# Performance work log

Hardware: AMD Instinct MI355X
Metric: run time of the kernel (lower is better)

## Reference

```python
import jax, jax.numpy as jnp
import numpy as np

DX, DY, MR, MBAR, NT, B, GOUT = 16, 8, 64, 256, 9, 4, 64
HX, EX, HRNN, HB = 1024, 512, 512, 2048
BB_IN = 1 + EX + HRNN


def setup_inputs() -> dict:
    key = jax.random.key(0)
    ks = jax.random.split(key, 12)
    total = (NT - 1) * MBAR + 1  # 2049 hidden-process time points
    X = jax.random.randint(ks[0], (B, total, DX), 0, 50).astype(jnp.float32)  # molecule counts
    Y = jax.random.normal(ks[1], (B, NT, DY), dtype=jnp.float32)
    # R: cumulative integrated reaction rates (non-decreasing in time)
    R = jnp.cumsum(jax.random.uniform(ks[2], (B, total, MR), dtype=jnp.float32) * 0.01, axis=1)
    stoich = (jax.random.randint(ks[3], (DX, MR), 0, 3) - 1).astype(jnp.float32)  # entries in {-1,0,1}
    times_t = jnp.linspace(0.0, 8.0, NT).astype(jnp.float32)
    times_tau = jnp.linspace(0.0, 1.0, MBAR).astype(jnp.float32)
    sc = lambda k, sh: jax.random.normal(k, sh, dtype=jnp.float32) * np.float32(1.0 / np.sqrt(sh[0]))
    Wx1, bx1 = sc(ks[4], (DX, HX)), jnp.zeros(HX, jnp.float32)
    Wx2, bx2 = sc(ks[5], (HX, EX)), jnp.zeros(EX, jnp.float32)
    Wih = sc(ks[6], (DY, HRNN))
    Whh = sc(ks[7], (HRNN, HRNN))
    bh = jnp.zeros(HRNN, jnp.float32)
    Wb1, bb1 = sc(ks[8], (BB_IN, HB)), jnp.zeros(HB, jnp.float32)
    Wb2, bb2 = sc(ks[9], (HB, GOUT)), jnp.zeros(GOUT, jnp.float32)
    return dict(X=X, Y=Y, R=R, stoich=stoich, times_t=times_t, times_tau=times_tau,
                Wx1=Wx1, bx1=bx1, Wx2=Wx2, bx2=bx2, Wih=Wih, Whh=Whh, bh=bh,
                Wb1=Wb1, bb1=bb1, Wb2=Wb2, bb2=bb2, k=1, k_prime=1, q=0, q_prime=1)


def reference(X, Y, R, stoich, times_t, times_tau,
              Wx1, bx1, Wx2, bx2, Wih, Whh, bh, Wb1, bb1, Wb2, bb2,
              k, k_prime, q, q_prime):
    """stochastic_integral_vectorized: gather displaced states, run the
    martingale network forward on base and displaced states, masked
    accumulation weighted by rate increments. Returns [GOUT]."""
    m_bar = times_tau.shape[0]
    base = k_prime * m_bar

    # --- Y encoder (Elman RNN over the observation slice, final hidden state) ---
    Yslice = Y[q, k + 1:, :]                       # [T_rem, DY]
    def rnn_step(h, y):
        return jnp.tanh(y @ Wih + h @ Whh + bh), None
    eY, _ = jax.lax.scan(rnn_step, jnp.zeros(Whh.shape[0], X.dtype), Yslice)  # [HRNN]

    # --- batched martingale forward: t [N], Xb [N, DX] -> [N, GOUT] ---
    def batched_forward(t, Xb):
        eX = jnp.tanh(Xb @ Wx1 + bx1) @ Wx2 + bx2          # [N, EX]
        eYb = jnp.broadcast_to(eY, (Xb.shape[0], eY.shape[0]))
        inp = jnp.concatenate([t[:, None], eX, eYb], axis=1)  # [N, 1+EX+HRNN]
        return jnp.tanh(inp @ Wb1 + bb1) @ Wb2 + bb2       # [N, GOUT]

    Xbase = X[q_prime, base:base + m_bar, :]               # [M_bar, DX]
    t = times_t[k] + times_tau                              # [M_bar]
    nn = batched_forward(t, Xbase)                          # [M_bar, GOUT]

    mr = stoich.shape[1]
    X_disp = Xbase[None, :, :] + stoich.T[:, None, :]       # [MR, M_bar, DX]
    valid = jnp.all(X_disp >= 0, axis=-1)                   # [MR, M_bar]
    nn_disp = batched_forward(jnp.tile(t, mr),
                              X_disp.reshape(mr * m_bar, -1)).reshape(mr, m_bar, -1)

    R_delta = R[q_prime, base + 1:base + m_bar + 1, :] - R[q_prime, base:base + m_bar, :]  # [M_bar, MR]
    si = jnp.einsum('jmg,mj,jm->g', nn_disp - nn[None], R_delta, valid.astype(nn.dtype))
    return si
```

## Files before the change

kernel.cpp:

```cpp
#include <hip/hip_runtime.h>
#include <math.h>

#define DXc   16
#define MRc   64
#define MBARc 256
#define NTc   9
#define DYc   8
#define HXc   1024
#define EXc   512
#define HRc   512
#define HBc   2048
#define GOUTc 64
#define TOTc  2049

using bf16x8 = __attribute__((ext_vector_type(8))) short;
using f32x4  = __attribute__((ext_vector_type(4))) float;

typedef unsigned int u32;
typedef u32 __attribute__((address_space(1))) gbl_u32;
typedef u32 __attribute__((address_space(3))) lds_u32;

__device__ __forceinline__ float fast_tanh(float x){
    float e = __expf(2.0f * x);
    return 1.0f - 2.0f / (e + 1.0f);
}

__device__ __forceinline__ short f2bf(float f){
    unsigned u = __builtin_bit_cast(unsigned, f);
    u = (u + 0x7FFFu + ((u >> 16) & 1u)) >> 16;
    return (short)u;
}

__device__ __forceinline__ void gld_lds16(const short* g, short* l){
    __builtin_amdgcn_global_load_lds((const gbl_u32*)g, (lds_u32*)l, 16, 0, 0);
}

__global__ void prep_kernel(const float* __restrict__ stoich, const float* __restrict__ Wx1,
                            const float* __restrict__ Wx2, const float* __restrict__ Wb1,
                            const float* __restrict__ X, const float* __restrict__ R,
                            const float* __restrict__ bx1, const float* __restrict__ bx2,
                            const int* kpptr, const int* qpptr,
                            float* __restrict__ SW, short* __restrict__ Wx2a,
                            short* __restrict__ Wb1p, float* __restrict__ XW,
                            float* __restrict__ T1, float* __restrict__ wrow,
                            float* __restrict__ hb0, float* __restrict__ dacc,
                            float* __restrict__ outz, float* __restrict__ eXb,
                            float* __restrict__ Z2Bacc, int* __restrict__ cnt){
    int b = blockIdx.x, tid = threadIdx.x;
    if (b < 256){
        int idx = b * 256 + tid;
        int j = idx >> 10, c = idx & 1023;
        float acc = 0.f;
        #pragma unroll
        for (int d = 0; d < DXc; ++d) acc += stoich[d * MRc + j] * Wx1[d * HXc + c];
        SW[idx] = acc;
    } else if (b < 512){
        size_t grp = (size_t)(b - 256) * 256 + tid;
        int lane = grp & 63;
        size_t t2 = grp >> 6;
        int kt = t2 & 15, mt = t2 >> 4;
        int c  = mt * 16 + (lane & 15);
        int e0 = kt * 32 + ((lane >> 4) << 3);
        short o8[8];
        #pragma unroll
        for (int jj = 0; jj < 8; ++jj) o8[jj] = f2bf(Wx2[(size_t)c * EXc + e0 + jj]);
        *(bf16x8*)(Wx2a + grp * 8) = *(bf16x8*)o8;
    } else if (b < 1024){
        size_t grp = (size_t)(b - 512) * 256 + tid;
        int lane = grp & 63;
        size_t t2 = grp >> 6;
        int kt = t2 & 15, nt = t2 >> 4;
        int n  = nt * 16 + (lane & 15);
        int k0 = kt * 32 + ((lane >> 4) << 3);
        short o8[8];
        #pragma unroll
        for (int jj = 0; jj < 8; ++jj) o8[jj] = f2bf(Wb1[(size_t)(1 + k0 + jj) * HBc + n]);
        *(bf16x8*)(Wb1p + grp * 8) = *(bf16x8*)o8;
    } else if (b < 2048){
        int idx = (b - 1024) * 256 + tid;
        int m = idx >> 10, c = idx & 1023;
        int base = kpptr[0] * MBARc;
        const float* xr = X + ((size_t)qpptr[0] * TOTc + base + m) * DXc;
        float acc = bx1[c];
        #pragma unroll
        for (int d = 0; d < DXc; ++d) acc += xr[d] * Wx1[d * HXc + c];
        XW[idx] = acc;
        T1[idx] = fast_tanh(acc);
    } else if (b < 2112){
        int j = b - 2048, m = tid;
        int base = kpptr[0] * MBARc;
        int qp = qpptr[0];
        const float* xr = X + ((size_t)qp * TOTc + base + m) * DXc;
        bool valid = true;
        #pragma unroll
        for (int d = 0; d < DXc; ++d) valid = valid && (xr[d] + stoich[d * MRc + j] >= 0.f);
        size_t rb = (size_t)qp * TOTc * MRc;
        float rd = R[rb + (size_t)(base + 1 + m) * MRc + j] - R[rb + (size_t)(base + m) * MRc + j];
        wrow[j * MBARc + m] = valid ? rd : 0.f;
    } else if (b == 2112){
        hb0[tid] = 0.f; hb0[tid + 256] = 0.f;
        #pragma unroll
        for (int l = 0; l < 8; ++l) dacc[tid + l * 256] = 0.f;
        if (tid < GOUTc) outz[tid] = 0.f;
        if (tid == 0) cnt[0] = 0;
    } else if (b < 2625){
        int idx = (b - 2113) * 256 + tid;
        eXb[idx] = bx2[idx & 511];
    } else {
        Z2Bacc[(size_t)(b - 2625) * 256 + tid] = 0.f;
    }
}

#define MMGRID(aa, bb) {                                                       \
    _Pragma("unroll") for (int i_ = 0; i_ < 4; ++i_)                           \
        _Pragma("unroll") for (int j_ = 0; j_ < 4; ++j_)                       \
            acc[i_][j_] = __builtin_amdgcn_mfma_f32_16x16x32_bf16(aa[i_], bb[j_], acc[i_][j_], 0, 0, 0); }

__device__ __forceinline__ void stage32(const short* __restrict__ Ap, const short* __restrict__ Bp,
                                        short* As, short* Bs,
                                        int at0, int bt0, int s, int KTOT, int wave, int lane){
    #pragma unroll
    for (int c = 0; c < 4; ++c){
        int ci = wave * 4 + c;
        int half = ci >> 3;
        int t    = ci & 7;
        const short* src = half ? (Bp + ((size_t)(bt0 + t) * KTOT + s) * 512 + lane * 8)
                                : (Ap + ((size_t)(at0 + t) * KTOT + s) * 512 + lane * 8);
        short* dst = (half ? Bs : As) + t * 512;
        gld_lds16(src, dst);
    }
}

#define STAGE_COMPUTE(As, Bs) {                                                       \
    bf16x8 af[4], bfr[4];                                                             \
    _Pragma("unroll") for (int i_ = 0; i_ < 4; ++i_)                                  \
        af[i_] = *(const bf16x8*)((As) + ((wm * 4 + i_) * 512) + lane * 8);           \
    _Pragma("unroll") for (int j_ = 0; j_ < 4; ++j_)                                  \
        bfr[j_] = *(const bf16x8*)((Bs) + ((wn * 4 + j_) * 512) + lane * 8);          \
    MMGRID(af, bfr); }

__global__ __launch_bounds__(256) void w12_act_ex_kernel(
    const short* __restrict__ Wx2a, const short* __restrict__ Wb1p,
    short* __restrict__ W12p,
    const float* __restrict__ XW, const float* __restrict__ T1,
    const float* __restrict__ SW, short* __restrict__ A1p,
    const float* __restrict__ Wx2, float* __restrict__ eXb){
    __shared__ __align__(16) short Asb[2][4096];
    __shared__ __align__(16) short Bsb[2][4096];
    int b = blockIdx.x, tid = threadIdx.x;
    if (b < 128){
        const int KTOT = 16, S = 16;
        int wave = tid >> 6, lane = tid & 63;
        int wm = wave >> 1, wn = wave & 1;
        int bx = b & 15, by = b >> 4;
        int quad = lane >> 4, llo = lane & 15;
        f32x4 acc[4][4];
        #pragma unroll
        for (int i = 0; i < 4; ++i)
            #pragma unroll
            for (int j = 0; j < 4; ++j) acc[i][j] = (f32x4){0.f, 0.f, 0.f, 0.f};
        stage32(Wx2a, Wb1p, Asb[0], Bsb[0], by * 8, bx * 8, 0, KTOT, wave, lane);
        for (int s = 0; s < S; ++s){
            int buf = s & 1;
            __syncthreads();
            if (s + 1 < S)
                stage32(Wx2a, Wb1p, Asb[buf ^ 1], Bsb[buf ^ 1], by * 8, bx * 8, s + 1, KTOT, wave, lane);
            STAGE_COMPUTE(Asb[buf], Bsb[buf]);
        }
        #pragma unroll
        for (int j = 0; j < 4; ++j){
            int h = bx * 128 + wn * 64 + j * 16 + llo;
            #pragma unroll
            for (int i = 0; i < 4; ++i){
                #pragma unroll
                for (int r = 0; r < 4; ++r){
                    int c = by * 128 + wm * 64 + i * 16 + quad * 4 + r;
                    W12p[(((size_t)(h >> 4) * 32 + (c >> 5)) * 64 + ((c & 31) >> 3) * 16 + llo) * 8 + (c & 7)] =
                        f2bf(acc[i][j][r]);
                }
            }
        }
    } else if (b < 8320){
        size_t grp = (size_t)(b - 128) * 256 + tid;
        int lane = grp & 63;
        size_t t2 = grp >> 6;
        int kt = t2 & 31;
        int mt = (int)(t2 >> 5);
        int m  = mt * 16 + (lane & 15);
        int c0 = kt * 32 + ((lane >> 4) << 3);
        int j    = m >> 8;
        int mloc = m & 255;
        const float* xwr = XW + (size_t)mloc * HXc + c0;
        const float* t1r = T1 + (size_t)mloc * HXc + c0;
        const float* swr = SW + (size_t)j * HXc + c0;
        short o8[8];
        #pragma unroll
        for (int i = 0; i < 8; ++i)
            o8[i] = f2bf(fast_tanh(xwr[i] + swr[i]) - t1r[i]);
        *(bf16x8*)(A1p + grp * 8) = *(bf16x8*)o8;
    } else {
        __shared__ float t1s[8 * 128];
        int bb = b - 8320;
        int mg = bb & 31, eh = (bb >> 5) & 1, kq = bb >> 6;
        int m0 = mg * 8, e = eh * 256 + tid, k0 = kq * 128;
        #pragma unroll
        for (int l = 0; l < 4; ++l){
            int idx = tid + l * 256;
            t1s[idx] = T1[(size_t)(m0 + (idx >> 7)) * HXc + k0 + (idx & 127)];
        }
        __syncthreads();
        float acc[8] = {};
        #pragma unroll 4
        for (int kk = 0; kk < 128; ++kk){
            float wv = Wx2[(size_t)(k0 + kk) * EXc + e];
            #pragma unroll
            for (int mm = 0; mm < 8; ++mm) acc[mm] += t1s[mm * 128 + kk] * wv;
        }
        #pragma unroll
        for (int mm = 0; mm < 8; ++mm)
            atomicAdd(&eXb[(size_t)(m0 + mm) * EXc + e], acc[mm]);
    }
}

__global__ __launch_bounds__(512) void rnn_cy_kernel(
    const float* __restrict__ Y, const float* __restrict__ Wih,
    const float* __restrict__ Whh, const float* __restrict__ bh,
    const float* __restrict__ Wb1, const float* __restrict__ bb1,
    const int* kptr, const int* qptr,
    float* __restrict__ hb0, float* __restrict__ hb1,
    int* __restrict__ cnt, float* __restrict__ cY){
    __shared__ float hs[HRc];
    __shared__ float psum[8][64];
    __shared__ float ps2[2][256];
    int tid = threadIdx.x;
    int o = tid & 63, seg = tid >> 6;
    int b = blockIdx.x;
    int out = b * 64 + o;
    int k = kptr[0], q = qptr[0];
    hs[tid] = 0.f;
    __syncthreads();
    for (int s = 0; s < 8; ++s){
        float* dst = (s & 1) ? hb0 : hb1;
        if (s > 0){
            const float* src = (s & 1) ? hb1 : hb0;
            if (tid == 0){
                int guard = 0;
                while (__hip_atomic_load(cnt, __ATOMIC_ACQUIRE, __HIP_MEMORY_SCOPE_AGENT) < 8 * s
                       && ++guard < (1 << 26)) {}
            }
            __syncthreads();
            hs[tid] = __hip_atomic_load(src + tid, __ATOMIC_RELAXED, __HIP_MEMORY_SCOPE_AGENT);
            __syncthreads();
        }
        int t = k + 1 + s;
        if (t < NTc){
            int k0 = seg * 64;
            float a0 = 0.f, a1 = 0.f, a2 = 0.f, a3 = 0.f;
            #pragma unroll 4
            for (int kk = 0; kk < 64; kk += 4){
                a0 += hs[k0 + kk + 0] * Whh[(size_t)(k0 + kk + 0) * HRc + out];
                a1 += hs[k0 + kk + 1] * Whh[(size_t)(k0 + kk + 1) * HRc + out];
                a2 += hs[k0 + kk + 2] * Whh[(size_t)(k0 + kk + 2) * HRc + out];
                a3 += hs[k0 + kk + 3] * Whh[(size_t)(k0 + kk + 3) * HRc + out];
            }
            psum[seg][o] = (a0 + a1) + (a2 + a3);
            __syncthreads();
            if (seg == 0){
                float a = 0.f;
                #pragma unroll
                for (int r = 0; r < 8; ++r) a += psum[r][o];
                const float* y = Y + (q * NTc + t) * DYc;
                float z = bh[out];
                #pragma unroll
                for (int d = 0; d < DYc; ++d) z += y[d] * Wih[d * HRc + out];
                __hip_atomic_store(dst + out, fast_tanh(z + a), __ATOMIC_RELEASE, __HIP_MEMORY_SCOPE_AGENT);
            }
            __syncthreads();
        } else {
            if (seg == 0)
                __hip_atomic_store(dst + out, hs[out], __ATOMIC_RELEASE, __HIP_MEMORY_SCOPE_AGENT);
            __syncthreads();
        }
        if (tid == 0)
            __hip_atomic_fetch_add(cnt, 1, __ATOMIC_RELEASE, __HIP_MEMORY_SCOPE_AGENT);
    }
    if (tid == 0){
        int guard = 0;
        while (__hip_atomic_load(cnt, __ATOMIC_ACQUIRE, __HIP_MEMORY_SCOPE_AGENT) < 64
               && ++guard < (1 << 26)) {}
    }
    __syncthreads();
    hs[tid] = __hip_atomic_load(hb0 + tid, __ATOMIC_RELAXED, __HIP_MEMORY_SCOPE_AGENT);
    __syncthreads();
    int o2 = tid & 255, sg = tid >> 8;
    int h = b * 256 + o2;
    float acc = 0.f;
    int e0 = sg * 256;
    #pragma unroll 4
    for (int e = 0; e < 256; ++e)
        acc += hs[e0 + e] * Wb1[(size_t)(1 + EXc + e0 + e) * HBc + h];
    ps2[sg][o2] = acc;
    __syncthreads();
    if (sg == 0)
        cY[h] = bb1[h] + ps2[0][o2] + ps2[1][o2];
}

__global__ __launch_bounds__(256) void z2acc_kernel(const float* __restrict__ eXb,
                                                    const float* __restrict__ Wb1,
                                                    float* __restrict__ Z2Bacc){
    __shared__ float exs[8 * 256];
    int b = blockIdx.x, tid = threadIdx.x;
    int mg = b & 31, hh = (b >> 5) & 7, kq = b >> 8;
    int m0 = mg * 8, h = hh * 256 + tid, k0 = kq * 256;
    #pragma unroll
    for (int l = 0; l < 8; ++l){
        int idx = tid + l * 256;
        exs[idx] = eXb[(size_t)(m0 + (idx >> 8)) * EXc + k0 + (idx & 255)];
    }
    __syncthreads();
    float acc[8] = {};
    #pragma unroll 4
    for (int kk = 0; kk < 256; ++kk){
        float wv = Wb1[(size_t)(1 + k0 + kk) * HBc + h];
        #pragma unroll
        for (int mm = 0; mm < 8; ++mm) acc[mm] += exs[mm * 256 + kk] * wv;
    }
    #pragma unroll
    for (int mm = 0; mm < 8; ++mm)
        atomicAdd(&Z2Bacc[(size_t)(m0 + mm) * HBc + h], acc[mm]);
}

__global__ void tb_kernel(const float* __restrict__ Z2Bacc, const float* __restrict__ Wb1,
                          const float* __restrict__ cY, const float* __restrict__ times_t,
                          const float* __restrict__ times_tau, const int* kptr,
                          float* __restrict__ TB){
    int b = blockIdx.x, tid = threadIdx.x;
    int m = b >> 3, h = (b & 7) * 256 + tid;
    float tk = times_t[kptr[0]];
    size_t idx = (size_t)m * HBc + h;
    float z = Z2Bacc[idx] + (tk + times_tau[m]) * Wb1[h] + cY[h];
    TB[idx] = fast_tanh(z);
}

__device__ __forceinline__ void stage24(const short* __restrict__ Ap, const short* __restrict__ Bp,
                                        short* As, short* Bs,
                                        int at0, int bt0, int s, int wave, int lane){
    #pragma unroll
    for (int c = 0; c < 6; ++c){
        int ci = wave * 6 + c;
        const short* src;
        short* dst;
        if (ci < 8){
            src = Ap + ((size_t)(at0 + ci) * 32 + s) * 512 + lane * 8;
            dst = As + ci * 512;
        } else {
            int t = ci - 8;
            src = Bp + ((size_t)(bt0 + t) * 32 + s) * 512 + lane * 8;
            dst = Bs + t * 512;
        }
        gld_lds16(src, dst);
    }
}

__global__ __launch_bounds__(256, 2) void gemm_big(
    const short* __restrict__ Ap, const short* __restrict__ Bp,
    const float* __restrict__ TB, const float* __restrict__ wrow,
    float* __restrict__ dacc){
    const int S = 32;
    __shared__ __align__(16) short Asb[2][4096];
    __shared__ __align__(16) short Bsb[2][8192];
    int tid = threadIdx.x;
    int wave = tid >> 6, lane = tid & 63;
    int wm = wave >> 1, wn = wave & 1;
    int bm = blockIdx.x, bn = blockIdx.y;
    int quad = lane >> 4, llo = lane & 15;
    f32x4 acc[4][8];
    #pragma unroll
    for (int i = 0; i < 4; ++i)
        #pragma unroll
        for (int j = 0; j < 8; ++j) acc[i][j] = (f32x4){0.f, 0.f, 0.f, 0.f};
    stage24(Ap, Bp, Asb[0], Bsb[0], bm * 8, bn * 16, 0, wave, lane);
    for (int s = 0; s < S; ++s){
        int buf = s & 1;
        __syncthreads();
        if (s + 1 < S)
            stage24(Ap, Bp, Asb[buf ^ 1], Bsb[buf ^ 1], bm * 8, bn * 16, s + 1, wave, lane);
        {
            bf16x8 af[4], bfr[8];
            #pragma unroll
            for (int i = 0; i < 4; ++i)
                af[i] = *(const bf16x8*)(Asb[buf] + ((wm * 4 + i) * 512) + lane * 8);
            #pragma unroll
            for (int j = 0; j < 8; ++j)
                bfr[j] = *(const bf16x8*)(Bsb[buf] + ((wn * 8 + j) * 512) + lane * 8);
            #pragma unroll
            for (int i = 0; i < 4; ++i)
                #pragma unroll
                for (int j = 0; j < 8; ++j)
                    acc[i][j] = __builtin_amdgcn_mfma_f32_16x16x32_bf16(af[i], bfr[j], acc[i][j], 0, 0, 0);
        }
    }
    int nj[8];
    #pragma unroll
    for (int j = 0; j < 8; ++j) nj[j] = bn * 256 + wn * 128 + j * 16 + llo;
    float part[8] = {};
    #pragma unroll
    for (int i = 0; i < 4; ++i){
        #pragma unroll
        for (int r = 0; r < 4; ++r){
            int m = bm * 128 + wm * 64 + i * 16 + quad * 4 + r;
            float wr = wrow[m];
            const float* trow = TB + (size_t)(m & 255) * HBc;
            #pragma unroll
            for (int j = 0; j < 8; ++j){
                float tb  = trow[nj[j]];
                float tdz = fast_tanh(acc[i][j][r]);
                float num = tdz * (1.0f - tb * tb);
                float den = 1.0f + tb * tdz;
                part[j] += wr * num * __builtin_amdgcn_rcpf(den);
            }
        }
    }
    #pragma unroll
    for (int j = 0; j < 8; ++j){
        part[j] += __shfl_xor(part[j], 16);
        part[j] += __shfl_xor(part[j], 32);
    }
    __shared__ float redn[256];
    redn[tid] = 0.f;
    __syncthreads();
    if (lane < 16){
        #pragma unroll
        for (int j = 0; j < 8; ++j)
            atomicAdd(&redn[wn * 128 + j * 16 + llo], part[j]);
    }
    __syncthreads();
    atomicAdd(&dacc[bn * 256 + tid], redn[tid]);
}

__global__ void out_kernel(const float* __restrict__ dacc, const float* __restrict__ Wb2,
                           float* __restrict__ out){
    __shared__ float red[4][64];
    int tid = threadIdx.x;
    int g = tid & 63, seg = tid >> 6;
    int h0 = blockIdx.x * 256 + seg * 64;
    float s = 0.f;
    #pragma unroll 8
    for (int hh = 0; hh < 64; ++hh)
        s += dacc[h0 + hh] * Wb2[(size_t)(h0 + hh) * GOUTc + g];
    red[seg][g] = s;
    __syncthreads();
    if (tid < 64)
        atomicAdd(&out[tid], red[0][tid] + red[1][tid] + red[2][tid] + red[3][tid]);
}

extern "C" void kernel_launch(void* const* d_in, const int* in_sizes, int n_in,
                              void* d_out, int out_size, void* d_ws, size_t ws_size,
                              hipStream_t stream){
    const float* X         = (const float*)d_in[0];
    const float* Y         = (const float*)d_in[1];
    const float* R         = (const float*)d_in[2];
    const float* stoich    = (const float*)d_in[3];
    const float* times_t   = (const float*)d_in[4];
    const float* times_tau = (const float*)d_in[5];
    const float* Wx1 = (const float*)d_in[6];
    const float* bx1 = (const float*)d_in[7];
    const float* Wx2 = (const float*)d_in[8];
    const float* bx2 = (const float*)d_in[9];
    const float* Wih = (const float*)d_in[10];
    const float* Whh = (const float*)d_in[11];
    const float* bh  = (const float*)d_in[12];
    const float* Wb1 = (const float*)d_in[13];
    const float* bb1 = (const float*)d_in[14];
    const float* Wb2 = (const float*)d_in[15];
    const int* kp  = (const int*)d_in[17];
    const int* kpp = (const int*)d_in[18];
    const int* qp  = (const int*)d_in[19];
    const int* qpp = (const int*)d_in[20];
    float* out = (float*)d_out;

    float* ws     = (float*)d_ws;
    float* hb0    = ws;
    float* hb1    = ws + 512;
    float* cY     = ws + 1024;
    float* dacc   = ws + 3072;
    float* wrow   = ws + 5120;
    float* SW     = ws + 21504;
    float* XW     = ws + 87040;
    float* T1     = ws + 349184;
    float* eXb    = ws + 611328;
    float* TB     = ws + 742400;
    float* Z2Bacc = ws + 1266688;
    short* A1p    = (short*)(ws + 1790976);
    short* Wx2a   = (short*)(ws + 10179584);
    short* Wb1p   = (short*)(ws + 10441728);
    short* W12p   = (short*)(ws + 10966016);
    int*   cnt    = (int*)(ws + 12014592);

    prep_kernel      <<<4673, 256, 0, stream>>>(stoich, Wx1, Wx2, Wb1, X, R, bx1, bx2, kpp, qpp,
                                                SW, Wx2a, Wb1p, XW, T1, wrow, hb0, dacc, out,
                                                eXb, Z2Bacc, cnt);
    w12_act_ex_kernel<<<8832, 256, 0, stream>>>(Wx2a, Wb1p, W12p, XW, T1, SW, A1p, Wx2, eXb);
    rnn_cy_kernel    <<<8,    512, 0, stream>>>(Y, Wih, Whh, bh, Wb1, bb1, kp, qp, hb0, hb1, cnt, cY);
    z2acc_kernel     <<<512,  256, 0, stream>>>(eXb, Wb1, Z2Bacc);
    tb_kernel        <<<2048, 256, 0, stream>>>(Z2Bacc, Wb1, cY, times_t, times_tau, kp, TB);
    gemm_big         <<<dim3(128, 8), 256, 0, stream>>>(A1p, W12p, TB, wrow, dacc);
    out_kernel       <<<8,    256, 0, stream>>>(dacc, Wb2, out);
}
```

Baseline: 293.5 us.

## Merge RNN/cY kernel into W12 and activation kernel, memset Z2Bacc, raise gemm occupancy

The serial RNN recurrence and cY projection now run as the first 8 blocks of a combined kernel that also does the W12 GEMM, the eX partial product and the A1 activation packing, so the latency-bound recurrence overlaps with that bulk work instead of running as its own launch. The eX block range moves ahead of A1 packing, Z2Bacc zeroing moves from prep_kernel blocks to hipMemsetAsync, and gemm_big's launch bounds ask for 3 blocks per CU. The RNN blocks spin on a global counter, so they depend on all 8 being resident together; putting them first in the grid makes that likely but not certain. The higher occupancy target may force register spills in gemm_big.

```diff
diff --git a/kernel.cpp b/kernel.cpp
--- a/kernel.cpp
+++ b/kernel.cpp
@@ -45,7 +45,7 @@
                             float* __restrict__ T1, float* __restrict__ wrow,
                             float* __restrict__ hb0, float* __restrict__ dacc,
                             float* __restrict__ outz, float* __restrict__ eXb,
-                            float* __restrict__ Z2Bacc, int* __restrict__ cnt){
+                            int* __restrict__ cnt){
     int b = blockIdx.x, tid = threadIdx.x;
     if (b < 256){
         int idx = b * 256 + tid;
@@ -103,11 +103,9 @@
         for (int l = 0; l < 8; ++l) dacc[tid + l * 256] = 0.f;
         if (tid < GOUTc) outz[tid] = 0.f;
         if (tid == 0) cnt[0] = 0;
-    } else if (b < 2625){
+    } else {
         int idx = (b - 2113) * 256 + tid;
         eXb[idx] = bx2[idx & 511];
-    } else {
-        Z2Bacc[(size_t)(b - 2625) * 256 + tid] = 0.f;
     }
 }
 
@@ -139,33 +137,113 @@
         bfr[j_] = *(const bf16x8*)((Bs) + ((wn * 4 + j_) * 512) + lane * 8);          \
     MMGRID(af, bfr); }
 
-__global__ __launch_bounds__(256) void w12_act_ex_kernel(
+__global__ __launch_bounds__(256) void mega2_kernel(
+    const float* __restrict__ Y, const float* __restrict__ Wih,
+    const float* __restrict__ Whh, const float* __restrict__ bh,
+    const float* __restrict__ Wb1, const float* __restrict__ bb1,
+    const int* kptr, const int* qptr,
+    float* __restrict__ hb0, float* __restrict__ hb1,
+    int* __restrict__ cnt, float* __restrict__ cY,
     const short* __restrict__ Wx2a, const short* __restrict__ Wb1p,
     short* __restrict__ W12p,
+    const float* __restrict__ Wx2, float* __restrict__ eXb,
     const float* __restrict__ XW, const float* __restrict__ T1,
-    const float* __restrict__ SW, short* __restrict__ A1p,
-    const float* __restrict__ Wx2, float* __restrict__ eXb){
-    __shared__ __align__(16) short Asb[2][4096];
-    __shared__ __align__(16) short Bsb[2][4096];
+    const float* __restrict__ SW, short* __restrict__ A1p){
+    __shared__ __align__(16) char smem[34816];
     int b = blockIdx.x, tid = threadIdx.x;
-    if (b < 128){
+    if (b < 8){
+        float* hs   = (float*)smem;
+        float (*psum)[64] = (float(*)[64])(smem + 2048);
+        int o = tid & 63, seg = tid >> 6;
+        int out = b * 64 + o;
+        int k = kptr[0], q = qptr[0];
+        hs[tid] = 0.f; hs[tid + 256] = 0.f;
+        __syncthreads();
+        for (int s = 0; s < 8; ++s){
+            float* dst = (s & 1) ? hb0 : hb1;
+            if (s > 0){
+                const float* src = (s & 1) ? hb1 : hb0;
+                if (tid == 0){
+                    int guard = 0;
+                    while (__hip_atomic_load(cnt, __ATOMIC_ACQUIRE, __HIP_MEMORY_SCOPE_AGENT) < 8 * s
+                           && ++guard < (1 << 26)) {}
+                }
+                __syncthreads();
+                hs[tid]       = __hip_atomic_load(src + tid,       __ATOMIC_RELAXED, __HIP_MEMORY_SCOPE_AGENT);
+                hs[tid + 256] = __hip_atomic_load(src + tid + 256, __ATOMIC_RELAXED, __HIP_MEMORY_SCOPE_AGENT);
+                __syncthreads();
+            }
+            int t = k + 1 + s;
+            if (t < NTc){
+                int k0 = seg * 128;
+                float a0 = 0.f, a1 = 0.f, a2 = 0.f, a3 = 0.f;
+                #pragma unroll 4
+                for (int kk = 0; kk < 128; kk += 4){
+                    a0 += hs[k0 + kk + 0] * Whh[(size_t)(k0 + kk + 0) * HRc + out];
+                    a1 += hs[k0 + kk + 1] * Whh[(size_t)(k0 + kk + 1) * HRc + out];
+                    a2 += hs[k0 + kk + 2] * Whh[(size_t)(k0 + kk + 2) * HRc + out];
+                    a3 += hs[k0 + kk + 3] * Whh[(size_t)(k0 + kk + 3) * HRc + out];
+                }
+                psum[seg][o] = (a0 + a1) + (a2 + a3);
+                __syncthreads();
+                if (seg == 0){
+                    float a = psum[0][o] + psum[1][o] + psum[2][o] + psum[3][o];
+                    const float* y = Y + (q * NTc + t) * DYc;
+                    float z = bh[out];
+                    #pragma unroll
+                    for (int d = 0; d < DYc; ++d) z += y[d] * Wih[d * HRc + out];
+                    __hip_atomic_store(dst + out, fast_tanh(z + a), __ATOMIC_RELEASE, __HIP_MEMORY_SCOPE_AGENT);
+                }
+                __syncthreads();
+            } else {
+                if (seg == 0)
+                    __hip_atomic_store(dst + out, hs[out], __ATOMIC_RELEASE, __HIP_MEMORY_SCOPE_AGENT);
+                __syncthreads();
+            }
+            if (tid == 0)
+                __hip_atomic_fetch_add(cnt, 1, __ATOMIC_RELEASE, __HIP_MEMORY_SCOPE_AGENT);
+        }
+        if (tid == 0){
+            int guard = 0;
+            while (__hip_atomic_load(cnt, __ATOMIC_ACQUIRE, __HIP_MEMORY_SCOPE_AGENT) < 64
+                   && ++guard < (1 << 26)) {}
+        }
+        __syncthreads();
+        hs[tid]       = __hip_atomic_load(hb0 + tid,       __ATOMIC_RELAXED, __HIP_MEMORY_SCOPE_AGENT);
+        hs[tid + 256] = __hip_atomic_load(hb0 + tid + 256, __ATOMIC_RELAXED, __HIP_MEMORY_SCOPE_AGENT);
+        __syncthreads();
+        int h = b * 256 + tid;
+        float acc = 0.f;
+        #pragma unroll 4
+        for (int e = 0; e < HRc; ++e)
+            acc += hs[e] * Wb1[(size_t)(1 + EXc + e) * HBc + h];
+        cY[h] = bb1[h] + acc;
+    } else if (b < 136){
+        short* As0 = (short*)smem;
+        short* As1 = (short*)(smem + 8192);
+        short* Bs0 = (short*)(smem + 16384);
+        short* Bs1 = (short*)(smem + 24576);
         const int KTOT = 16, S = 16;
         int wave = tid >> 6, lane = tid & 63;
         int wm = wave >> 1, wn = wave & 1;
-        int bx = b & 15, by = b >> 4;
+        int b2 = b - 8;
+        int bx = b2 & 15, by = b2 >> 4;
         int quad = lane >> 4, llo = lane & 15;
         f32x4 acc[4][4];
         #pragma unroll
         for (int i = 0; i < 4; ++i)
             #pragma unroll
             for (int j = 0; j < 4; ++j) acc[i][j] = (f32x4){0.f, 0.f, 0.f, 0.f};
-        stage32(Wx2a, Wb1p, Asb[0], Bsb[0], by * 8, bx * 8, 0, KTOT, wave, lane);
+        stage32(Wx2a, Wb1p, As0, Bs0, by * 8, bx * 8, 0, KTOT, wave, lane);
         for (int s = 0; s < S; ++s){
-            int buf = s & 1;
+            short* Asc = (s & 1) ? As1 : As0;
+            short* Bsc = (s & 1) ? Bs1 : Bs0;
+            short* Asn = (s & 1) ? As0 : As1;
+            short* Bsn = (s & 1) ? Bs0 : Bs1;
             __syncthreads();
             if (s + 1 < S)
-                stage32(Wx2a, Wb1p, Asb[buf ^ 1], Bsb[buf ^ 1], by * 8, bx * 8, s + 1, KTOT, wave, lane);
-            STAGE_COMPUTE(Asb[buf], Bsb[buf]);
+                stage32(Wx2a, Wb1p, Asn, Bsn, by * 8, bx * 8, s + 1, KTOT, wave, lane);
+            STAGE_COMPUTE(Asc, Bsc);
         }
         #pragma unroll
         for (int j = 0; j < 4; ++j){
@@ -180,8 +258,29 @@
                 }
             }
         }
-    } else if (b < 8320){
-        size_t grp = (size_t)(b - 128) * 256 + tid;
+    } else if (b < 648){
+        float* t1s = (float*)smem;
+        int bb = b - 136;
+        int mg = bb & 31, eh = (bb >> 5) & 1, kq = bb >> 6;
+        int m0 = mg * 8, e = eh * 256 + tid, k0 = kq * 128;
+        #pragma unroll
+        for (int l = 0; l < 4; ++l){
+            int idx = tid + l * 256;
+            t1s[idx] = T1[(size_t)(m0 + (idx >> 7)) * HXc + k0 + (idx & 127)];
+        }
+        __syncthreads();
+        float acc[8] = {};
+        #pragma unroll 4
+        for (int kk = 0; kk < 128; ++kk){
+            float wv = Wx2[(size_t)(k0 + kk) * EXc + e];
+            #pragma unroll
+            for (int mm = 0; mm < 8; ++mm) acc[mm] += t1s[mm * 128 + kk] * wv;
+        }
+        #pragma unroll
+        for (int mm = 0; mm < 8; ++mm)
+            atomicAdd(&eXb[(size_t)(m0 + mm) * EXc + e], acc[mm]);
+    } else {
+        size_t grp = (size_t)(b - 648) * 256 + tid;
         int lane = grp & 63;
         size_t t2 = grp >> 6;
         int kt = t2 & 31;
@@ -198,111 +297,7 @@
         for (int i = 0; i < 8; ++i)
             o8[i] = f2bf(fast_tanh(xwr[i] + swr[i]) - t1r[i]);
         *(bf16x8*)(A1p + grp * 8) = *(bf16x8*)o8;
-    } else {
-        __shared__ float t1s[8 * 128];
-        int bb = b - 8320;
-        int mg = bb & 31, eh = (bb >> 5) & 1, kq = bb >> 6;
-        int m0 = mg * 8, e = eh * 256 + tid, k0 = kq * 128;
-        #pragma unroll
-        for (int l = 0; l < 4; ++l){
-            int idx = tid + l * 256;
-            t1s[idx] = T1[(size_t)(m0 + (idx >> 7)) * HXc + k0 + (idx & 127)];
-        }
-        __syncthreads();
-        float acc[8] = {};
-        #pragma unroll 4
-        for (int kk = 0; kk < 128; ++kk){
-            float wv = Wx2[(size_t)(k0 + kk) * EXc + e];
-            #pragma unroll
-            for (int mm = 0; mm < 8; ++mm) acc[mm] += t1s[mm * 128 + kk] * wv;
-        }
-        #pragma unroll
-        for (int mm = 0; mm < 8; ++mm)
-            atomicAdd(&eXb[(size_t)(m0 + mm) * EXc + e], acc[mm]);
-    }
-}
-
-__global__ __launch_bounds__(512) void rnn_cy_kernel(
-    const float* __restrict__ Y, const float* __restrict__ Wih,
-    const float* __restrict__ Whh, const float* __restrict__ bh,
-    const float* __restrict__ Wb1, const float* __restrict__ bb1,
-    const int* kptr, const int* qptr,
-    float* __restrict__ hb0, float* __restrict__ hb1,
-    int* __restrict__ cnt, float* __restrict__ cY){
-    __shared__ float hs[HRc];
-    __shared__ float psum[8][64];
-    __shared__ float ps2[2][256];
-    int tid = threadIdx.x;
-    int o = tid & 63, seg = tid >> 6;
-    int b = blockIdx.x;
-    int out = b * 64 + o;
-    int k = kptr[0], q = qptr[0];
-    hs[tid] = 0.f;
-    __syncthreads();
-    for (int s = 0; s < 8; ++s){
-        float* dst = (s & 1) ? hb0 : hb1;
-        if (s > 0){
-            const float* src = (s & 1) ? hb1 : hb0;
-            if (tid == 0){
-                int guard = 0;
-                while (__hip_atomic_load(cnt, __ATOMIC_ACQUIRE, __HIP_MEMORY_SCOPE_AGENT) < 8 * s
-                       && ++guard < (1 << 26)) {}
-            }
-            __syncthreads();
-            hs[tid] = __hip_atomic_load(src + tid, __ATOMIC_RELAXED, __HIP_MEMORY_SCOPE_AGENT);
-            __syncthreads();
-        }
-        int t = k + 1 + s;
-        if (t < NTc){
-            int k0 = seg * 64;
-            float a0 = 0.f, a1 = 0.f, a2 = 0.f, a3 = 0.f;
-            #pragma unroll 4
-            for (int kk = 0; kk < 64; kk += 4){
-                a0 += hs[k0 + kk + 0] * Whh[(size_t)(k0 + kk + 0) * HRc + out];
-                a1 += hs[k0 + kk + 1] * Whh[(size_t)(k0 + kk + 1) * HRc + out];
-                a2 += hs[k0 + kk + 2] * Whh[(size_t)(k0 + kk + 2) * HRc + out];
-                a3 += hs[k0 + kk + 3] * Whh[(size_t)(k0 + kk + 3) * HRc + out];
-            }
-            psum[seg][o] = (a0 + a1) + (a2 + a3);
-            __syncthreads();
-            if (seg == 0){
-                float a = 0.f;
-                #pragma unroll
-                for (int r = 0; r < 8; ++r) a += psum[r][o];
-                const float* y = Y + (q * NTc + t) * DYc;
-                float z = bh[out];
-                #pragma unroll
-                for (int d = 0; d < DYc; ++d) z += y[d] * Wih[d * HRc + out];
-                __hip_atomic_store(dst + out, fast_tanh(z + a), __ATOMIC_RELEASE, __HIP_MEMORY_SCOPE_AGENT);
-            }
-            __syncthreads();
-        } else {
-            if (seg == 0)
-                __hip_atomic_store(dst + out, hs[out], __ATOMIC_RELEASE, __HIP_MEMORY_SCOPE_AGENT);
-            __syncthreads();
-        }
-        if (tid == 0)
-            __hip_atomic_fetch_add(cnt, 1, __ATOMIC_RELEASE, __HIP_MEMORY_SCOPE_AGENT);
-    }
-    if (tid == 0){
-        int guard = 0;
-        while (__hip_atomic_load(cnt, __ATOMIC_ACQUIRE, __HIP_MEMORY_SCOPE_AGENT) < 64
-               && ++guard < (1 << 26)) {}
-    }
-    __syncthreads();
-    hs[tid] = __hip_atomic_load(hb0 + tid, __ATOMIC_RELAXED, __HIP_MEMORY_SCOPE_AGENT);
-    __syncthreads();
-    int o2 = tid & 255, sg = tid >> 8;
-    int h = b * 256 + o2;
-    float acc = 0.f;
-    int e0 = sg * 256;
-    #pragma unroll 4
-    for (int e = 0; e < 256; ++e)
-        acc += hs[e0 + e] * Wb1[(size_t)(1 + EXc + e0 + e) * HBc + h];
-    ps2[sg][o2] = acc;
-    __syncthreads();
-    if (sg == 0)
-        cY[h] = bb1[h] + ps2[0][o2] + ps2[1][o2];
+    }
 }
 
 __global__ __launch_bounds__(256) void z2acc_kernel(const float* __restrict__ eXb,
@@ -362,7 +357,7 @@
     }
 }
 
-__global__ __launch_bounds__(256, 2) void gemm_big(
+__global__ __launch_bounds__(256, 3) void gemm_big(
     const short* __restrict__ Ap, const short* __restrict__ Bp,
     const float* __restrict__ TB, const float* __restrict__ wrow,
     float* __restrict__ dacc){
@@ -497,13 +492,14 @@
     short* W12p   = (short*)(ws + 10966016);
     int*   cnt    = (int*)(ws + 12014592);
 
-    prep_kernel      <<<4673, 256, 0, stream>>>(stoich, Wx1, Wx2, Wb1, X, R, bx1, bx2, kpp, qpp,
-                                                SW, Wx2a, Wb1p, XW, T1, wrow, hb0, dacc, out,
-                                                eXb, Z2Bacc, cnt);
-    w12_act_ex_kernel<<<8832, 256, 0, stream>>>(Wx2a, Wb1p, W12p, XW, T1, SW, A1p, Wx2, eXb);
-    rnn_cy_kernel    <<<8,    512, 0, stream>>>(Y, Wih, Whh, bh, Wb1, bb1, kp, qp, hb0, hb1, cnt, cY);
-    z2acc_kernel     <<<512,  256, 0, stream>>>(eXb, Wb1, Z2Bacc);
-    tb_kernel        <<<2048, 256, 0, stream>>>(Z2Bacc, Wb1, cY, times_t, times_tau, kp, TB);
-    gemm_big         <<<dim3(128, 8), 256, 0, stream>>>(A1p, W12p, TB, wrow, dacc);
-    out_kernel       <<<8,    256, 0, stream>>>(dacc, Wb2, out);
-}
+    hipMemsetAsync(Z2Bacc, 0, (size_t)MBARc * HBc * sizeof(float), stream);
+    prep_kernel  <<<2625, 256, 0, stream>>>(stoich, Wx1, Wx2, Wb1, X, R, bx1, bx2, kpp, qpp,
+                                            SW, Wx2a, Wb1p, XW, T1, wrow, hb0, dacc, out,
+                                            eXb, cnt);
+    mega2_kernel <<<8840, 256, 0, stream>>>(Y, Wih, Whh, bh, Wb1, bb1, kp, qp, hb0, hb1, cnt, cY,
+                                            Wx2a, Wb1p, W12p, Wx2, eXb, XW, T1, SW, A1p);
+    z2acc_kernel <<<512,  256, 0, stream>>>(eXb, Wb1, Z2Bacc);
+    tb_kernel    <<<2048, 256, 0, stream>>>(Z2Bacc, Wb1, cY, times_t, times_tau, kp, TB);
+    gemm_big     <<<dim3(128, 8), 256, 0, stream>>>(A1p, W12p, TB, wrow, dacc);
+    out_kernel   <<<8,    256, 0, stream>>>(dacc, Wb2, out);
+}
```

New measurement: 430.7 us. 46.8% more time.
